# Kernel optimization log

Measured on AMD Instinct MI355X. Metric: run time of the kernel, lower is better.

## Reference

```python
import math
import jax, jax.numpy as jnp
import numpy as np

C = 64
GRID = 2

def _conv1x1(x, W, b):
    # 1x1 conv == channel-mixing matmul: [B,C,H,W] x [O,C] -> [B,O,H,W]
    return jnp.einsum('bchw,oc->bohw', x, W) + b[None, :, None, None]

def setup_inputs() -> dict:
    key = jax.random.key(0)
    ks = jax.random.split(key, 11)
    s = 1.0 / math.sqrt(C)
    def w(k):
        return jax.random.normal(k, (C, C), dtype=jnp.float32) * s
    def bias(k):
        return jax.random.normal(k, (C,), dtype=jnp.float32) * 0.02
    return {
        'x': jax.random.normal(ks[0], (2, C, 128, 128), dtype=jnp.float32),
        'Wq': w(ks[1]), 'bq': bias(ks[2]),
        'Wk': w(ks[3]), 'bk': bias(ks[4]),
        'Wa': w(ks[5]), 'ba': bias(ks[6]),
        'Wb': w(ks[7]), 'bb': bias(ks[8]),
        'Wo': w(ks[9]), 'bo': bias(ks[10]),
    }

def reference(x, Wq, bq, Wk, bk, Wa, ba, Wb, bb, Wo, bo):
    B, c, H, W = x.shape
    g = GRID
    rh, rw = H // g, W // g  # H,W chosen divisible by grid -> no reflect pad
    N = rh * rw
    R = g * g

    q = _conv1x1(x, Wq, bq)
    k = _conv1x1(x, Wk, bk)
    a = _conv1x1(x, Wa, ba)
    bt = _conv1x1(x, Wb, bb)

    def regionize(t):
        # [B,C,H,W] -> [B, R, C, N] with N = rh*rw row-major per region
        return t.reshape(B, c, g, rh, g, rw).transpose(0, 2, 4, 1, 3, 5).reshape(B, R, c, N)

    qr, kr, ar, br = regionize(q), regionize(k), regionize(a), regionize(bt)

    # attn[b,r,n,m] = softmax_m( q^T k / sqrt(C) )
    attn = jax.nn.softmax(jnp.einsum('brcn,brcm->brnm', qr, kr) / math.sqrt(c), axis=-1)

    # out_r = alpha @ attn + beta @ attn^T
    out = (jnp.einsum('brcj,brjm->brcm', ar, attn)
           + jnp.einsum('brcj,brmj->brcm', br, attn))

    # [B,R,C,N] -> [B,C,H,W]
    out = out.reshape(B, g, g, c, rh, rw).transpose(0, 3, 1, 4, 2, 5).reshape(B, c, H, W)
    return _conv1x1(out, Wo, bo)
```

## Files before the change

kernel.cpp:

```cpp
#include <hip/hip_runtime.h>


typedef __attribute__((ext_vector_type(8)))  short bf16x8;
typedef __attribute__((ext_vector_type(16))) float f32x16;

#define MFMA32(a, b, c) __builtin_amdgcn_mfma_f32_32x32x16_bf16(a, b, c, 0, 0, 0)

constexpr int REG_ELEMS = 4096 * 64;
constexpr size_t QP_OFF    = 0;
constexpr size_t KP_OFF    = 4u  << 20;
constexpr size_t ATL_OFF   = 8u  << 20;
constexpr size_t BTL_OFF   = 12u << 20;
constexpr size_t OUTP_OFF  = 16u << 20;
constexpr size_t LNV_OFF   = 20u << 20;
constexpr size_t LPART_OFF = (20u << 20) + (128u << 10);

constexpr float QSCALE = 0.18033688011112042f;

__device__ __forceinline__ short f2bf(float f) {
    union { float f; unsigned u; } v; v.f = f;
    unsigned r = v.u + 0x7fffu + ((v.u >> 16) & 1u);
    return (short)(r >> 16);
}
__device__ __forceinline__ float bf2f(short s) {
    union { unsigned u; float f; } v; v.u = ((unsigned)(unsigned short)s) << 16;
    return v.f;
}
__device__ __forceinline__ unsigned fbits(float f) {
    union { float f; unsigned u; } v; v.f = f; return v.u;
}
__device__ __forceinline__ unsigned pack_trunc(float e0, float e1) {
    return __builtin_amdgcn_perm(fbits(e1), fbits(e0), 0x07060302u);
}
__device__ __forceinline__ f32x16 zero16() {
    f32x16 z;
    #pragma unroll
    for (int i = 0; i < 16; ++i) z[i] = 0.f;
    return z;
}
__device__ __forceinline__ float fexp2(float x) {
#if __has_builtin(__builtin_amdgcn_exp2f)
    return __builtin_amdgcn_exp2f(x);
#else
    return exp2f(x);
#endif
}
__device__ __forceinline__ void permswap32(unsigned& a, unsigned& b, bool hi) {
#if __has_builtin(__builtin_amdgcn_permlane32_swap)
    auto r = __builtin_amdgcn_permlane32_swap(a, b, false, false);
    a = r[0]; b = r[1];
#elif __has_builtin(__builtin_amdgcn_permlane32_swap_b32)
    auto r = __builtin_amdgcn_permlane32_swap_b32(a, b, false, false);
    a = r[0]; b = r[1];
#else
    unsigned ax = (unsigned)__shfl_xor((int)a, 32);
    unsigned bx = (unsigned)__shfl_xor((int)b, 32);
    unsigned na = hi ? bx : a;
    unsigned nb = hi ? b  : ax;
    a = na; b = nb;
#endif
}

typedef __attribute__((address_space(1))) const unsigned char as1_t;
typedef __attribute__((address_space(3))) unsigned char as3_t;
__device__ __forceinline__ void stage16(const void* g, void* l) {
    __builtin_amdgcn_global_load_lds((as1_t*)g, (as3_t*)l, 16, 0, 0);
}

__global__ __launch_bounds__(256) void k_conv_in(
    const float* __restrict__ x,
    const float* __restrict__ Wq, const float* __restrict__ bq,
    const float* __restrict__ Wk, const float* __restrict__ bk,
    const float* __restrict__ Wa, const float* __restrict__ ba,
    const float* __restrict__ Wb, const float* __restrict__ bb,
    char* __restrict__ ws)
{
    const int tid  = threadIdx.x;
    const int blk  = blockIdx.x;
    const int wseg = blk & 1;
    const int h    = (blk >> 1) & 127;
    const int b    = blk >> 8;
    const int br   = b * 4 + (h >> 6) * 2 + wseg;
    const int n0   = (h & 63) * 64;

    __shared__ float xs[64][68];
    __shared__ short trans[2][64][72];

    const float* xp = x + ((size_t)b * 64 * 16384) + (size_t)h * 128 + wseg * 64;
    #pragma unroll
    for (int r = 0; r < 4; ++r) {
        int idx = r * 256 + tid;
        int c   = idx >> 4;
        int w4  = (idx & 15) << 2;
        *(float4*)&xs[c][w4] = *(const float4*)(xp + (size_t)c * 16384 + w4);
    }
    __syncthreads();

    const int lane = tid & 63;
    const int wid  = tid >> 6;
    const int col  = lane & 31;
    const int l5   = lane >> 5;
    const int pH   = wid & 1;
    const int oH   = wid >> 1;
    const int px   = pH * 32 + col;
    const int oc   = oH * 32 + col;

    bf16x8 xhi[4], xlo[4];
    #pragma unroll
    for (int s = 0; s < 4; ++s) {
        union { bf16x8 v; short sh[8]; } uh, ul;
        #pragma unroll
        for (int e = 0; e < 8; ++e) {
            float xv = xs[s * 16 + l5 * 8 + e][px];
            short hh = f2bf(xv);
            uh.sh[e] = hh;
            ul.sh[e] = f2bf(xv - bf2f(hh));
        }
        xhi[s] = uh.v; xlo[s] = ul.v;
    }

    #pragma unroll
    for (int mat = 0; mat < 4; ++mat) {
        const float* Wsel = (mat == 0) ? Wq : (mat == 1) ? Wk : (mat == 2) ? Wa : Wb;
        const float* bsel = (mat == 0) ? bq : (mat == 1) ? bk : (mat == 2) ? ba : bb;

        bf16x8 whi[4], wlo[4];
        const float* wrow = Wsel + (size_t)oc * 64;
        #pragma unroll
        for (int s = 0; s < 4; ++s) {
            float4 f0 = *(const float4*)(wrow + s * 16 + l5 * 8);
            float4 f1 = *(const float4*)(wrow + s * 16 + l5 * 8 + 4);
            float wf[8] = { f0.x, f0.y, f0.z, f0.w, f1.x, f1.y, f1.z, f1.w };
            union { bf16x8 v; short sh[8]; } uh, ul;
            #pragma unroll
            for (int e = 0; e < 8; ++e) {
                short hh = f2bf(wf[e]);
                uh.sh[e] = hh;
                ul.sh[e] = f2bf(wf[e] - bf2f(hh));
            }
            whi[s] = uh.v; wlo[s] = ul.v;
        }

        f32x16 d = zero16();
        #pragma unroll
        for (int s = 0; s < 4; ++s) {
            d = MFMA32(xhi[s], whi[s], d);
            d = MFMA32(xhi[s], wlo[s], d);
            d = MFMA32(xlo[s], whi[s], d);
        }

        const float bias = bsel[oc];
        if (mat < 2) {
            const float sc = (mat == 0) ? QSCALE : 1.0f;
            #pragma unroll
            for (int r = 0; r < 16; ++r) {
                int pxl = pH * 32 + (r & 3) + 8 * (r >> 2) + 4 * l5;
                trans[mat][pxl][oc] = f2bf((d[r] + bias) * sc);
            }
        } else {
            short* base = (short*)(ws + (mat == 2 ? ATL_OFF : BTL_OFF))
                          + (size_t)br * REG_ELEMS;
            const int sw   = (oc >> 1) & 3;
            const int tile = (n0 >> 5) + pH;
            #pragma unroll
            for (int q = 0; q < 4; ++q) {
                short tmp4[4];
                #pragma unroll
                for (int rr = 0; rr < 4; ++rr) tmp4[rr] = f2bf(d[4 * q + rr] + bias);
                int segp = q ^ sw;
                short* p = base + (size_t)tile * 2048 + oc * 32 + segp * 8 + 4 * l5;
                *(uint2*)p = *(uint2*)tmp4;
            }
        }
    }
    __syncthreads();

    #pragma unroll
    for (int rep = 0; rep < 4; ++rep) {
        int idx  = rep * 256 + tid;
        int mat2 = idx >> 9;
        int row  = (idx >> 3) & 63;
        int seg  = idx & 7;
        short* dst = (short*)(ws + (mat2 ? KP_OFF : QP_OFF))
                     + (size_t)br * REG_ELEMS + (size_t)(n0 + row) * 64
                     + (seg ^ (row & 7)) * 8;
        *(uint4*)dst = *(uint4*)&trans[mat2][row][seg * 8];
    }
}

__global__ __launch_bounds__(256, 2) void k_stats(char* __restrict__ ws)
{
    const int tid  = threadIdx.x;
    const int br   = blockIdx.x & 7;
    const int nt   = (blockIdx.x >> 3) & 63;
    const int ms   = blockIdx.x >> 9;
    const int lane = tid & 63;
    const int w    = tid >> 6;
    const int wn   = w & 1;
    const int wi   = w >> 1;
    const int col  = lane & 31;
    const int l5   = lane >> 5;

    const short* Qb  = (const short*)(ws + QP_OFF) + (size_t)br * REG_ELEMS;
    const char*  Kbb = ws + KP_OFF + (size_t)br * REG_ELEMS * 2
                       + (size_t)ms * 262144;

    __shared__ __align__(16) char smem[16896];

    const int nrow = nt * 64 + wn * 32 + col;
    bf16x8 afr[4];
    #pragma unroll
    for (int s = 0; s < 4; ++s)
        afr[s] = *(const bf16x8*)(Qb + (size_t)nrow * 64 + (((2*s+l5) ^ (col & 7)) * 8));

    float sm[16];
    #pragma unroll
    for (int r = 0; r < 16; ++r) sm[r] = 0.f;

    {
        const char* g = Kbb + (size_t)w * 2048 + lane * 16;
        char* l = smem + w * 2048;
        stage16(g, l); stage16(g + 1024, l + 1024);
    }

    #pragma unroll 2
    for (int slab = 0; slab < 32; ++slab) {
        __syncthreads();
        if (slab + 1 < 32) {
            const char* g = Kbb + (size_t)(slab + 1) * 8192 + w * 2048 + lane * 16;
            char* l = smem + ((slab + 1) & 1) * 8192 + w * 2048;
            stage16(g, l); stage16(g + 1024, l + 1024);
        }
        const short* Ks = (const short*)(smem + (slab & 1) * 8192);
        f32x16 d = zero16();
        #pragma unroll
        for (int s = 0; s < 4; ++s) {
            bf16x8 bf = *(const bf16x8*)(Ks + (wi * 32 + col) * 64
                                         + ((2*s+l5) ^ (col & 7)) * 8);
            d = MFMA32(afr[s], bf, d);
        }
        #pragma unroll
        for (int r = 0; r < 16; ++r) sm[r] += fexp2(d[r]);
    }

    #pragma unroll
    for (int off = 1; off < 32; off <<= 1)
        #pragma unroll
        for (int r = 0; r < 16; ++r) sm[r] += __shfl_xor(sm[r], off);

    __syncthreads();
    float* Lred = (float*)(smem + 16384);
    if (col == 0) {
        #pragma unroll
        for (int r = 0; r < 16; ++r)
            Lred[w * 32 + ((r & 3) + 8 * (r >> 2) + 4 * l5)] = sm[r];
    }
    __syncthreads();
    if (tid < 64) {
        int wn2 = tid >> 5, nl = tid & 31;
        float L = Lred[wn2 * 32 + nl] + Lred[(wn2 + 2) * 32 + nl];
        ((float*)(ws + LPART_OFF))[(size_t)ms * 32768 + (size_t)br * 4096
                                   + nt * 64 + tid] = L;
    }
}

__global__ __launch_bounds__(256) void k_ascale(char* __restrict__ ws)
{
    const int tid = threadIdx.x;
    const int br  = blockIdx.x & 7;
    const int nt  = blockIdx.x >> 3;

    __shared__ float Larr[64];

    if (tid < 64) {
        const float* Lp = (const float*)(ws + LPART_OFF);
        const size_t idx = (size_t)br * 4096 + nt * 64 + tid;
        float li = 1.0f / (Lp[idx] + Lp[32768 + idx]);
        Larr[tid] = li;
        ((float*)(ws + LNV_OFF))[idx] = li;
    }
    __syncthreads();

    short* Ab = (short*)(ws + ATL_OFF) + (size_t)br * REG_ELEMS + (size_t)nt * 4096;
    #pragma unroll
    for (int rep = 0; rep < 2; ++rep) {
        int id = rep * 256 + tid;
        int t = id >> 8, c = (id >> 2) & 63, s = id & 3;
        int sg = s ^ ((c >> 1) & 3);
        int jl = t * 32 + sg * 8;
        short* p = Ab + (size_t)t * 2048 + c * 32 + s * 8;
        uint4 v = *(uint4*)p;
        short* sp = (short*)&v;
        short o[8];
        #pragma unroll
        for (int e = 0; e < 8; ++e) o[e] = f2bf(bf2f(sp[e]) * Larr[jl + e]);
        *(uint4*)p = *(uint4*)o;
    }
}

__global__ __launch_bounds__(256, 2) void k_attn(char* __restrict__ ws)
{
    const int tid  = threadIdx.x;
    const int br   = blockIdx.x & 7;
    const int mt   = blockIdx.x >> 3;
    const int lane = tid & 63;
    const int w    = tid >> 6;
    const int wj   = w & 1;
    const int jsw  = w >> 1;
    const int col  = lane & 31;
    const int l5   = lane >> 5;
    const bool hi  = (l5 != 0);

    const char* Qbb = ws + QP_OFF  + (size_t)br * REG_ELEMS * 2;
    const char* Kbb = ws + KP_OFF  + (size_t)br * REG_ELEMS * 2;
    const char* Abb = ws + ATL_OFF + (size_t)br * REG_ELEMS * 2;
    const char* Bbb = ws + BTL_OFF + (size_t)br * REG_ELEMS * 2;
    const float* Lnv = (const float*)(ws + LNV_OFF) + (size_t)br * 4096;
    short* OutPb    = (short*)(ws + OUTP_OFF) + (size_t)br * REG_ELEMS;

    __shared__ __align__(16) char smem[65536];

    const short* msrcb = (const short*)(wj == 0 ? Kbb : Qbb);
    bf16x8 mf[2][4];
    #pragma unroll
    for (int h = 0; h < 2; ++h) {
        const short* mr = msrcb + (size_t)(mt * 64 + h * 32 + col) * 64;
        #pragma unroll
        for (int s = 0; s < 4; ++s)
            mf[h][s] = *(const bf16x8*)(mr + ((2*s+l5) ^ (col & 7)) * 8);
    }

    f32x16 acc00 = zero16(), acc01 = zero16();
    f32x16 acc10 = zero16(), acc11 = zero16();

    const char* gsb = (w == 0) ? Qbb : (w == 1) ? Kbb : (w == 2) ? Abb : Bbb;

    {
        #pragma unroll
        for (int h = 0; h < 2; ++h) {
            const char* g = gsb + (size_t)h * 262144 + lane * 16;
            char* l = smem + h * 16384 + w * 4096 + lane * 16;
            #pragma unroll
            for (int i = 0; i < 4; ++i) stage16(g + i * 1024, l + i * 1024);
        }
    }

    #pragma unroll 2
    for (int rnd = 0; rnd < 64; ++rnd) {
        __syncthreads();
        if (rnd + 1 < 64) {
            #pragma unroll
            for (int h = 0; h < 2; ++h) {
                const char* g = gsb + (size_t)h * 262144
                                + (size_t)(rnd + 1) * 4096 + lane * 16;
                char* l = smem + ((rnd + 1) & 1) * 32768 + h * 16384
                          + w * 4096 + lane * 16;
                #pragma unroll
                for (int i = 0; i < 4; ++i) stage16(g + i * 1024, l + i * 1024);
            }
        }
        const char* sb = smem + (rnd & 1) * 32768 + jsw * 16384;
        const short* jr = (const short*)(sb + (wj == 0 ? 0 : 4096));
        const short* ts = (const short*)(sb + (wj == 0 ? 8192 : 12288));

        bf16x8 a[4];
        #pragma unroll
        for (int s = 0; s < 4; ++s)
            a[s] = *(const bf16x8*)(jr + col * 64 + ((2*s+l5) ^ (col & 7)) * 8);

        f32x16 d0 = zero16(), d1 = zero16();
        #pragma unroll
        for (int s = 0; s < 4; ++s) {
            d0 = MFMA32(a[s], mf[0][s], d0);
            d1 = MFMA32(a[s], mf[1][s], d1);
        }

        unsigned W0[8], W1[8];
        #pragma unroll
        for (int q = 0; q < 4; ++q) {
            W0[2*q]   = pack_trunc(fexp2(d0[4*q]),   fexp2(d0[4*q+1]));
            W0[2*q+1] = pack_trunc(fexp2(d0[4*q+2]), fexp2(d0[4*q+3]));
            W1[2*q]   = pack_trunc(fexp2(d1[4*q]),   fexp2(d1[4*q+1]));
            W1[2*q+1] = pack_trunc(fexp2(d1[4*q+2]), fexp2(d1[4*q+3]));
        }

        #pragma unroll
        for (int k16 = 0; k16 < 2; ++k16) {
            unsigned u0 = W0[4*k16+0], u1 = W0[4*k16+1];
            unsigned u2 = W0[4*k16+2], u3 = W0[4*k16+3];
            permswap32(u0, u2, hi);
            permswap32(u1, u3, hi);
            union { uint4 u; bf16x8 v; } fr0;
            fr0.u.x = u0; fr0.u.y = u1; fr0.u.z = u2; fr0.u.w = u3;

            unsigned v0 = W1[4*k16+0], v1 = W1[4*k16+1];
            unsigned v2 = W1[4*k16+2], v3 = W1[4*k16+3];
            permswap32(v0, v2, hi);
            permswap32(v1, v3, hi);
            union { uint4 u; bf16x8 v; } fr1;
            fr1.u.x = v0; fr1.u.y = v1; fr1.u.z = v2; fr1.u.w = v3;

            const int swz = ((2*k16 + l5) ^ ((col >> 1) & 3)) * 8;
            bf16x8 bL = *(const bf16x8*)(ts + col * 32 + swz);
            bf16x8 bH = *(const bf16x8*)(ts + (col + 32) * 32 + swz);
            acc00 = MFMA32(fr0.v, bL, acc00);
            acc01 = MFMA32(fr0.v, bH, acc01);
            acc10 = MFMA32(fr1.v, bL, acc10);
            acc11 = MFMA32(fr1.v, bH, acc11);
        }
    }

    __syncthreads();
    float* red = (float*)smem;
    if (w == 0) {
        #pragma unroll
        for (int h = 0; h < 2; ++h)
            #pragma unroll
            for (int r = 0; r < 16; ++r) {
                int ml = h * 32 + (r & 3) + 8 * (r >> 2) + 4 * l5;
                red[ml * 68 + col]      = h ? acc10[r] : acc00[r];
                red[ml * 68 + 32 + col] = h ? acc11[r] : acc01[r];
            }
    }
    __syncthreads();
    if (w == 2) {
        #pragma unroll
        for (int h = 0; h < 2; ++h)
            #pragma unroll
            for (int r = 0; r < 16; ++r) {
                int ml = h * 32 + (r & 3) + 8 * (r >> 2) + 4 * l5;
                red[ml * 68 + col]      += h ? acc10[r] : acc00[r];
                red[ml * 68 + 32 + col] += h ? acc11[r] : acc01[r];
            }
    }
    __syncthreads();
    if (w == 1) {
        #pragma unroll
        for (int h = 0; h < 2; ++h)
            #pragma unroll
            for (int r = 0; r < 16; ++r) {
                int ml = h * 32 + (r & 3) + 8 * (r >> 2) + 4 * l5;
                float li = Lnv[mt * 64 + ml];
                red[ml * 68 + col]      += li * (h ? acc10[r] : acc00[r]);
                red[ml * 68 + 32 + col] += li * (h ? acc11[r] : acc01[r]);
            }
    }
    __syncthreads();
    if (w == 3) {
        #pragma unroll
        for (int h = 0; h < 2; ++h)
            #pragma unroll
            for (int r = 0; r < 16; ++r) {
                int ml = h * 32 + (r & 3) + 8 * (r >> 2) + 4 * l5;
                float li = Lnv[mt * 64 + ml];
                red[ml * 68 + col]      += li * (h ? acc10[r] : acc00[r]);
                red[ml * 68 + 32 + col] += li * (h ? acc11[r] : acc01[r]);
            }
    }
    __syncthreads();
    {
        const int m  = tid >> 2;
        const int c0 = (tid & 3) * 16;
        const float* rp = red + m * 68 + c0;
        uint4 p0, p1;
        p0.x = pack_trunc(rp[0],  rp[1]);  p0.y = pack_trunc(rp[2],  rp[3]);
        p0.z = pack_trunc(rp[4],  rp[5]);  p0.w = pack_trunc(rp[6],  rp[7]);
        p1.x = pack_trunc(rp[8],  rp[9]);  p1.y = pack_trunc(rp[10], rp[11]);
        p1.z = pack_trunc(rp[12], rp[13]); p1.w = pack_trunc(rp[14], rp[15]);
        short* orow = OutPb + (size_t)(mt * 64 + m) * 64 + c0;
        *(uint4*)orow       = p0;
        *(uint4*)(orow + 8) = p1;
    }
}

__global__ __launch_bounds__(256) void k_conv_out(
    const char* __restrict__ ws,
    const float* __restrict__ Wo, const float* __restrict__ bo,
    float* __restrict__ out)
{
    const int tid  = threadIdx.x;
    const int lane = tid & 63;
    const int sub  = tid >> 6;
    const int blk  = blockIdx.x;
    const int br   = blk & 7;
    const int nt   = (blk >> 3) * 4 + sub;
    const int col  = lane & 31;
    const int l5   = lane >> 5;

    const short* OutPb = (const short*)(ws + OUTP_OFF) + (size_t)br * REG_ELEMS;

    bf16x8 afr[4];
    const short* arow = OutPb + (size_t)(nt * 32 + col) * 64 + l5 * 8;
    #pragma unroll
    for (int s = 0; s < 4; ++s) afr[s] = *(const bf16x8*)(arow + s * 16);

    bf16x8 bw[2][4];
    #pragma unroll
    for (int oh = 0; oh < 2; ++oh) {
        const float* wrow = Wo + (size_t)(oh * 32 + col) * 64 + l5 * 8;
        #pragma unroll
        for (int s = 0; s < 4; ++s) {
            float4 f0 = *(const float4*)(wrow + s * 16);
            float4 f1 = *(const float4*)(wrow + s * 16 + 4);
            union { bf16x8 v; short sh[8]; } u;
            u.sh[0] = f2bf(f0.x); u.sh[1] = f2bf(f0.y);
            u.sh[2] = f2bf(f0.z); u.sh[3] = f2bf(f0.w);
            u.sh[4] = f2bf(f1.x); u.sh[5] = f2bf(f1.y);
            u.sh[6] = f2bf(f1.z); u.sh[7] = f2bf(f1.w);
            bw[oh][s] = u.v;
        }
    }

    f32x16 d0 = zero16(), d1 = zero16();
    #pragma unroll
    for (int s = 0; s < 4; ++s) {
        d0 = MFMA32(afr[s], bw[0][s], d0);
        d1 = MFMA32(afr[s], bw[1][s], d1);
    }

    const int b  = br >> 2;
    const int gi = (br >> 1) & 1;
    const int gj = br & 1;

    #pragma unroll
    for (int oh = 0; oh < 2; ++oh) {
        const int oc = oh * 32 + col;
        const float bias = bo[oc];
        const f32x16& d = oh ? d1 : d0;
        #pragma unroll
        for (int q = 0; q < 4; ++q) {
            int nloc = 8 * q + 4 * l5;
            int nreg = nt * 32 + nloc;
            int wp   = nreg & 63;
            int ip   = nreg >> 6;
            float4 v = make_float4(d[4*q+0] + bias, d[4*q+1] + bias,
                                   d[4*q+2] + bias, d[4*q+3] + bias);
            float* op = out + ((size_t)(b * 64 + oc)) * 16384
                        + (size_t)(gi * 64 + ip) * 128 + gj * 64 + wp;
            *(float4*)op = v;
        }
    }
}

extern "C" void kernel_launch(void* const* d_in, const int* in_sizes, int n_in,
                              void* d_out, int out_size, void* d_ws, size_t ws_size,
                              hipStream_t stream)
{
    const float* x  = (const float*)d_in[0];
    const float* Wq = (const float*)d_in[1];
    const float* bq = (const float*)d_in[2];
    const float* Wk = (const float*)d_in[3];
    const float* bk = (const float*)d_in[4];
    const float* Wa = (const float*)d_in[5];
    const float* ba = (const float*)d_in[6];
    const float* Wb = (const float*)d_in[7];
    const float* bb = (const float*)d_in[8];
    const float* Wo = (const float*)d_in[9];
    const float* bo = (const float*)d_in[10];
    char* ws   = (char*)d_ws;
    float* out = (float*)d_out;

    hipLaunchKernelGGL(k_conv_in,  dim3(512),  dim3(256), 0, stream,
                       x, Wq, bq, Wk, bk, Wa, ba, Wb, bb, ws);
    hipLaunchKernelGGL(k_stats,    dim3(1024), dim3(256), 0, stream, ws);
    hipLaunchKernelGGL(k_ascale,   dim3(512),  dim3(256), 0, stream, ws);
    hipLaunchKernelGGL(k_attn,     dim3(512),  dim3(256), 0, stream, ws);
    hipLaunchKernelGGL(k_conv_out, dim3(256),  dim3(256), 0, stream,
                       ws, Wo, bo, out);
}
```

Measured before the change: 202.2 us.

## Split attention j-range across two blocks and widen m-tile to 128

Each attention block now covers 128 output rows (four 32-row halves) instead of 64, and the j reduction is split in two across blocks, each writing its own bf16 partial output buffer. The output 1x1 conv then sums the two partial buffers by running extra MFMAs over both. The aim is to reuse each staged K/Q/A/B tile across more rows, halving shared-memory staging traffic per unit of work while keeping the grid size the same. In exchange it needs more accumulator registers (eight f32x16 accumulators), which may reduce occupancy or cause spills under launch_bounds(256,2). It also adds a second partial buffer with an extra bf16 rounding step before the final sum.

```diff
diff --git a/kernel.cpp b/kernel.cpp
--- a/kernel.cpp
+++ b/kernel.cpp
@@ -11,9 +11,10 @@
 constexpr size_t KP_OFF    = 4u  << 20;
 constexpr size_t ATL_OFF   = 8u  << 20;
 constexpr size_t BTL_OFF   = 12u << 20;
-constexpr size_t OUTP_OFF  = 16u << 20;
-constexpr size_t LNV_OFF   = 20u << 20;
-constexpr size_t LPART_OFF = (20u << 20) + (128u << 10);
+constexpr size_t OUTP0_OFF = 16u << 20;
+constexpr size_t OUTP1_OFF = 20u << 20;
+constexpr size_t LNV_OFF   = 24u << 20;
+constexpr size_t LPART_OFF = (24u << 20) + (128u << 10);
 
 constexpr float QSCALE = 0.18033688011112042f;
 
@@ -302,7 +303,8 @@
 {
     const int tid  = threadIdx.x;
     const int br   = blockIdx.x & 7;
-    const int mt   = blockIdx.x >> 3;
+    const int mt   = (blockIdx.x >> 3) & 31;
+    const int js   = blockIdx.x >> 8;
     const int lane = tid & 63;
     const int w    = tid >> 6;
     const int wj   = w & 1;
@@ -316,44 +318,48 @@
     const char* Abb = ws + ATL_OFF + (size_t)br * REG_ELEMS * 2;
     const char* Bbb = ws + BTL_OFF + (size_t)br * REG_ELEMS * 2;
     const float* Lnv = (const float*)(ws + LNV_OFF) + (size_t)br * 4096;
-    short* OutPb    = (short*)(ws + OUTP_OFF) + (size_t)br * REG_ELEMS;
+    short* OutPb = (short*)(ws + (js ? OUTP1_OFF : OUTP0_OFF)) + (size_t)br * REG_ELEMS;
 
     __shared__ __align__(16) char smem[65536];
 
     const short* msrcb = (const short*)(wj == 0 ? Kbb : Qbb);
-    bf16x8 mf[2][4];
-    #pragma unroll
-    for (int h = 0; h < 2; ++h) {
-        const short* mr = msrcb + (size_t)(mt * 64 + h * 32 + col) * 64;
+    bf16x8 mf[4][4];
+    #pragma unroll
+    for (int h = 0; h < 4; ++h) {
+        const short* mr = msrcb + (size_t)(mt * 128 + h * 32 + col) * 64;
         #pragma unroll
         for (int s = 0; s < 4; ++s)
             mf[h][s] = *(const bf16x8*)(mr + ((2*s+l5) ^ (col & 7)) * 8);
     }
 
-    f32x16 acc00 = zero16(), acc01 = zero16();
-    f32x16 acc10 = zero16(), acc11 = zero16();
-
-    const char* gsb = (w == 0) ? Qbb : (w == 1) ? Kbb : (w == 2) ? Abb : Bbb;
+    f32x16 acc[4][2];
+    #pragma unroll
+    for (int h = 0; h < 4; ++h) {
+        acc[h][0] = zero16();
+        acc[h][1] = zero16();
+    }
+
+    const char* gsb = ((w == 0) ? Qbb : (w == 1) ? Kbb : (w == 2) ? Abb : Bbb)
+                      + (size_t)js * 262144;
 
     {
         #pragma unroll
-        for (int h = 0; h < 2; ++h) {
-            const char* g = gsb + (size_t)h * 262144 + lane * 16;
-            char* l = smem + h * 16384 + w * 4096 + lane * 16;
+        for (int h2 = 0; h2 < 2; ++h2) {
+            const char* g = gsb + (size_t)h2 * 4096 + lane * 16;
+            char* l = smem + h2 * 16384 + w * 4096 + lane * 16;
             #pragma unroll
             for (int i = 0; i < 4; ++i) stage16(g + i * 1024, l + i * 1024);
         }
     }
 
     #pragma unroll 2
-    for (int rnd = 0; rnd < 64; ++rnd) {
+    for (int rnd = 0; rnd < 32; ++rnd) {
         __syncthreads();
-        if (rnd + 1 < 64) {
-            #pragma unroll
-            for (int h = 0; h < 2; ++h) {
-                const char* g = gsb + (size_t)h * 262144
-                                + (size_t)(rnd + 1) * 4096 + lane * 16;
-                char* l = smem + ((rnd + 1) & 1) * 32768 + h * 16384
+        if (rnd + 1 < 32) {
+            #pragma unroll
+            for (int h2 = 0; h2 < 2; ++h2) {
+                const char* g = gsb + (size_t)(2 * (rnd + 1) + h2) * 4096 + lane * 16;
+                char* l = smem + ((rnd + 1) & 1) * 32768 + h2 * 16384
                           + w * 4096 + lane * 16;
                 #pragma unroll
                 for (int i = 0; i < 4; ++i) stage16(g + i * 1024, l + i * 1024);
@@ -361,52 +367,42 @@
         }
         const char* sb = smem + (rnd & 1) * 32768 + jsw * 16384;
         const short* jr = (const short*)(sb + (wj == 0 ? 0 : 4096));
-        const short* ts = (const short*)(sb + (wj == 0 ? 8192 : 12288));
+        const short* ts = (const short*)(sb + 8192 + wj * 4096);
 
         bf16x8 a[4];
         #pragma unroll
         for (int s = 0; s < 4; ++s)
             a[s] = *(const bf16x8*)(jr + col * 64 + ((2*s+l5) ^ (col & 7)) * 8);
 
-        f32x16 d0 = zero16(), d1 = zero16();
-        #pragma unroll
-        for (int s = 0; s < 4; ++s) {
-            d0 = MFMA32(a[s], mf[0][s], d0);
-            d1 = MFMA32(a[s], mf[1][s], d1);
-        }
-
-        unsigned W0[8], W1[8];
-        #pragma unroll
-        for (int q = 0; q < 4; ++q) {
-            W0[2*q]   = pack_trunc(fexp2(d0[4*q]),   fexp2(d0[4*q+1]));
-            W0[2*q+1] = pack_trunc(fexp2(d0[4*q+2]), fexp2(d0[4*q+3]));
-            W1[2*q]   = pack_trunc(fexp2(d1[4*q]),   fexp2(d1[4*q+1]));
-            W1[2*q+1] = pack_trunc(fexp2(d1[4*q+2]), fexp2(d1[4*q+3]));
+        unsigned W[4][8];
+        #pragma unroll
+        for (int h = 0; h < 4; ++h) {
+            f32x16 d = zero16();
+            #pragma unroll
+            for (int s = 0; s < 4; ++s) d = MFMA32(a[s], mf[h][s], d);
+            #pragma unroll
+            for (int q = 0; q < 4; ++q) {
+                W[h][2*q]   = pack_trunc(fexp2(d[4*q]),   fexp2(d[4*q+1]));
+                W[h][2*q+1] = pack_trunc(fexp2(d[4*q+2]), fexp2(d[4*q+3]));
+            }
         }
 
         #pragma unroll
         for (int k16 = 0; k16 < 2; ++k16) {
-            unsigned u0 = W0[4*k16+0], u1 = W0[4*k16+1];
-            unsigned u2 = W0[4*k16+2], u3 = W0[4*k16+3];
-            permswap32(u0, u2, hi);
-            permswap32(u1, u3, hi);
-            union { uint4 u; bf16x8 v; } fr0;
-            fr0.u.x = u0; fr0.u.y = u1; fr0.u.z = u2; fr0.u.w = u3;
-
-            unsigned v0 = W1[4*k16+0], v1 = W1[4*k16+1];
-            unsigned v2 = W1[4*k16+2], v3 = W1[4*k16+3];
-            permswap32(v0, v2, hi);
-            permswap32(v1, v3, hi);
-            union { uint4 u; bf16x8 v; } fr1;
-            fr1.u.x = v0; fr1.u.y = v1; fr1.u.z = v2; fr1.u.w = v3;
-
             const int swz = ((2*k16 + l5) ^ ((col >> 1) & 3)) * 8;
             bf16x8 bL = *(const bf16x8*)(ts + col * 32 + swz);
             bf16x8 bH = *(const bf16x8*)(ts + (col + 32) * 32 + swz);
-            acc00 = MFMA32(fr0.v, bL, acc00);
-            acc01 = MFMA32(fr0.v, bH, acc01);
-            acc10 = MFMA32(fr1.v, bL, acc10);
-            acc11 = MFMA32(fr1.v, bH, acc11);
+            #pragma unroll
+            for (int h = 0; h < 4; ++h) {
+                unsigned u0 = W[h][4*k16+0], u1 = W[h][4*k16+1];
+                unsigned u2 = W[h][4*k16+2], u3 = W[h][4*k16+3];
+                permswap32(u0, u2, hi);
+                permswap32(u1, u3, hi);
+                union { uint4 u; bf16x8 v; } fr;
+                fr.u.x = u0; fr.u.y = u1; fr.u.z = u2; fr.u.w = u3;
+                acc[h][0] = MFMA32(fr.v, bL, acc[h][0]);
+                acc[h][1] = MFMA32(fr.v, bH, acc[h][1]);
+            }
         }
     }
 
@@ -414,62 +410,64 @@
     float* red = (float*)smem;
     if (w == 0) {
         #pragma unroll
-        for (int h = 0; h < 2; ++h)
+        for (int h = 0; h < 4; ++h)
             #pragma unroll
             for (int r = 0; r < 16; ++r) {
                 int ml = h * 32 + (r & 3) + 8 * (r >> 2) + 4 * l5;
-                red[ml * 68 + col]      = h ? acc10[r] : acc00[r];
-                red[ml * 68 + 32 + col] = h ? acc11[r] : acc01[r];
+                red[ml * 68 + col]      = acc[h][0][r];
+                red[ml * 68 + 32 + col] = acc[h][1][r];
             }
     }
     __syncthreads();
     if (w == 2) {
         #pragma unroll
-        for (int h = 0; h < 2; ++h)
+        for (int h = 0; h < 4; ++h)
             #pragma unroll
             for (int r = 0; r < 16; ++r) {
                 int ml = h * 32 + (r & 3) + 8 * (r >> 2) + 4 * l5;
-                red[ml * 68 + col]      += h ? acc10[r] : acc00[r];
-                red[ml * 68 + 32 + col] += h ? acc11[r] : acc01[r];
+                red[ml * 68 + col]      += acc[h][0][r];
+                red[ml * 68 + 32 + col] += acc[h][1][r];
             }
     }
     __syncthreads();
     if (w == 1) {
         #pragma unroll
-        for (int h = 0; h < 2; ++h)
+        for (int h = 0; h < 4; ++h)
             #pragma unroll
             for (int r = 0; r < 16; ++r) {
                 int ml = h * 32 + (r & 3) + 8 * (r >> 2) + 4 * l5;
-                float li = Lnv[mt * 64 + ml];
-                red[ml * 68 + col]      += li * (h ? acc10[r] : acc00[r]);
-                red[ml * 68 + 32 + col] += li * (h ? acc11[r] : acc01[r]);
+                float li = Lnv[mt * 128 + ml];
+                red[ml * 68 + col]      += li * acc[h][0][r];
+                red[ml * 68 + 32 + col] += li * acc[h][1][r];
             }
     }
     __syncthreads();
     if (w == 3) {
         #pragma unroll
-        for (int h = 0; h < 2; ++h)
+        for (int h = 0; h < 4; ++h)
             #pragma unroll
             for (int r = 0; r < 16; ++r) {
                 int ml = h * 32 + (r & 3) + 8 * (r >> 2) + 4 * l5;
-                float li = Lnv[mt * 64 + ml];
-                red[ml * 68 + col]      += li * (h ? acc10[r] : acc00[r]);
-                red[ml * 68 + 32 + col] += li * (h ? acc11[r] : acc01[r]);
+                float li = Lnv[mt * 128 + ml];
+                red[ml * 68 + col]      += li * acc[h][0][r];
+                red[ml * 68 + 32 + col] += li * acc[h][1][r];
             }
     }
     __syncthreads();
     {
-        const int m  = tid >> 2;
-        const int c0 = (tid & 3) * 16;
+        const int m  = tid >> 1;
+        const int c0 = (tid & 1) * 32;
         const float* rp = red + m * 68 + c0;
-        uint4 p0, p1;
-        p0.x = pack_trunc(rp[0],  rp[1]);  p0.y = pack_trunc(rp[2],  rp[3]);
-        p0.z = pack_trunc(rp[4],  rp[5]);  p0.w = pack_trunc(rp[6],  rp[7]);
-        p1.x = pack_trunc(rp[8],  rp[9]);  p1.y = pack_trunc(rp[10], rp[11]);
-        p1.z = pack_trunc(rp[12], rp[13]); p1.w = pack_trunc(rp[14], rp[15]);
-        short* orow = OutPb + (size_t)(mt * 64 + m) * 64 + c0;
-        *(uint4*)orow       = p0;
-        *(uint4*)(orow + 8) = p1;
+        short* orow = OutPb + (size_t)(mt * 128 + m) * 64 + c0;
+        #pragma unroll
+        for (int g4 = 0; g4 < 4; ++g4) {
+            uint4 pk;
+            pk.x = pack_trunc(rp[8*g4 + 0], rp[8*g4 + 1]);
+            pk.y = pack_trunc(rp[8*g4 + 2], rp[8*g4 + 3]);
+            pk.z = pack_trunc(rp[8*g4 + 4], rp[8*g4 + 5]);
+            pk.w = pack_trunc(rp[8*g4 + 6], rp[8*g4 + 7]);
+            *(uint4*)(orow + g4 * 8) = pk;
+        }
     }
 }
 
@@ -487,12 +485,16 @@
     const int col  = lane & 31;
     const int l5   = lane >> 5;
 
-    const short* OutPb = (const short*)(ws + OUTP_OFF) + (size_t)br * REG_ELEMS;
-
-    bf16x8 afr[4];
-    const short* arow = OutPb + (size_t)(nt * 32 + col) * 64 + l5 * 8;
-    #pragma unroll
-    for (int s = 0; s < 4; ++s) afr[s] = *(const bf16x8*)(arow + s * 16);
+    const short* O0 = (const short*)(ws + OUTP0_OFF) + (size_t)br * REG_ELEMS;
+    const short* O1 = (const short*)(ws + OUTP1_OFF) + (size_t)br * REG_ELEMS;
+
+    bf16x8 af0[4], af1[4];
+    const size_t aoff = (size_t)(nt * 32 + col) * 64 + l5 * 8;
+    #pragma unroll
+    for (int s = 0; s < 4; ++s) {
+        af0[s] = *(const bf16x8*)(O0 + aoff + s * 16);
+        af1[s] = *(const bf16x8*)(O1 + aoff + s * 16);
+    }
 
     bf16x8 bw[2][4];
     #pragma unroll
@@ -514,8 +516,10 @@
     f32x16 d0 = zero16(), d1 = zero16();
     #pragma unroll
     for (int s = 0; s < 4; ++s) {
-        d0 = MFMA32(afr[s], bw[0][s], d0);
-        d1 = MFMA32(afr[s], bw[1][s], d1);
+        d0 = MFMA32(af0[s], bw[0][s], d0);
+        d0 = MFMA32(af1[s], bw[0][s], d0);
+        d1 = MFMA32(af0[s], bw[1][s], d1);
+        d1 = MFMA32(af1[s], bw[1][s], d1);
     }
 
     const int b  = br >> 2;
```

New measurement: 217.0 us. 7.3% more time.

## Give each wave a private staging buffer and drop the per-round block barrier

Applied to the files above, without the earlier changes.

Each wave now stages only the J and T slabs it consumes into its own double-buffered LDS region, instead of all waves cooperatively staging shared tiles. The per-iteration __syncthreads is replaced by an explicit vmcnt waitcnt on that wave's own async loads. This removes block-wide barrier stalls and lets waves run decoupled. The risks are that the slab indexing (2*(rnd+1)+jsw) must match the old data mapping, and that the waitcnt encodings must correctly cover the LDS-direct loads before they are read.

```diff
diff --git a/kernel.cpp b/kernel.cpp
--- a/kernel.cpp
+++ b/kernel.cpp
@@ -333,35 +333,39 @@
     f32x16 acc00 = zero16(), acc01 = zero16();
     f32x16 acc10 = zero16(), acc11 = zero16();
 
-    const char* gsb = (w == 0) ? Qbb : (w == 1) ? Kbb : (w == 2) ? Abb : Bbb;
+    const char* gj = (wj == 0) ? Qbb : Kbb;
+    const char* gt = (wj == 0) ? Abb : Bbb;
+    char* myb = smem + w * 16384;
 
     {
-        #pragma unroll
-        for (int h = 0; h < 2; ++h) {
-            const char* g = gsb + (size_t)h * 262144 + lane * 16;
-            char* l = smem + h * 16384 + w * 4096 + lane * 16;
-            #pragma unroll
-            for (int i = 0; i < 4; ++i) stage16(g + i * 1024, l + i * 1024);
-        }
+        const char* gjs = gj + (size_t)jsw * 4096 + lane * 16;
+        const char* gts = gt + (size_t)jsw * 4096 + lane * 16;
+        char* l = myb + lane * 16;
+        #pragma unroll
+        for (int i = 0; i < 4; ++i) stage16(gjs + i * 1024, l + i * 1024);
+        #pragma unroll
+        for (int i = 0; i < 4; ++i) stage16(gts + i * 1024, l + 4096 + i * 1024);
     }
 
     #pragma unroll 2
     for (int rnd = 0; rnd < 64; ++rnd) {
-        __syncthreads();
         if (rnd + 1 < 64) {
-            #pragma unroll
-            for (int h = 0; h < 2; ++h) {
-                const char* g = gsb + (size_t)h * 262144
-                                + (size_t)(rnd + 1) * 4096 + lane * 16;
-                char* l = smem + ((rnd + 1) & 1) * 32768 + h * 16384
-                          + w * 4096 + lane * 16;
-                #pragma unroll
-                for (int i = 0; i < 4; ++i) stage16(g + i * 1024, l + i * 1024);
-            }
-        }
-        const char* sb = smem + (rnd & 1) * 32768 + jsw * 16384;
-        const short* jr = (const short*)(sb + (wj == 0 ? 0 : 4096));
-        const short* ts = (const short*)(sb + (wj == 0 ? 8192 : 12288));
+            const int slab = 2 * (rnd + 1) + jsw;
+            const char* gjs = gj + (size_t)slab * 4096 + lane * 16;
+            const char* gts = gt + (size_t)slab * 4096 + lane * 16;
+            char* l = myb + ((rnd + 1) & 1) * 8192 + lane * 16;
+            #pragma unroll
+            for (int i = 0; i < 4; ++i) stage16(gjs + i * 1024, l + i * 1024);
+            #pragma unroll
+            for (int i = 0; i < 4; ++i) stage16(gts + i * 1024, l + 4096 + i * 1024);
+            __builtin_amdgcn_s_waitcnt(0x0F78);
+        } else {
+            __builtin_amdgcn_s_waitcnt(0x0F70);
+        }
+
+        const char* sb = myb + (rnd & 1) * 8192;
+        const short* jr = (const short*)sb;
+        const short* ts = (const short*)(sb + 4096);
 
         bf16x8 a[4];
         #pragma unroll
```

After: 204.3 us. No clear change (+1.0%).
